# Kernel tuning notes

Measured on AMD Instinct MI355X. Metric: run time of the kernel, lower is better.

The kernel has to match this reference:

```python
import jax, jax.numpy as jnp
import numpy as np

N, E = 20000, 320000
IN, HID, R, HEADS = 128, 256, 4, 4
C = HID // HEADS  # per-head dim


def setup_inputs() -> dict:
    key = jax.random.key(0)
    ks = jax.random.split(key, 20)
    g = lambda k, s, sc=0.05: jax.random.normal(k, s, jnp.float32) * sc
    return {
        'x': g(ks[0], (N, IN), 1.0),
        'edge_index': jax.random.randint(ks[1], (2, E), 0, N),
        'edge_type': jax.random.randint(ks[2], (E,), 0, R),
        'h_prev': g(ks[3], (N, HID), 1.0),
        # RGCN layer 1: relation weights, root weight, bias
        'W1': g(ks[4], (R, IN, HID)), 'root1': g(ks[5], (IN, HID)), 'b1': jnp.zeros((HID,), jnp.float32),
        # RGCN layer 2
        'W2': g(ks[6], (R, HID, HID)), 'root2': g(ks[7], (HID, HID)), 'b2': jnp.zeros((HID,), jnp.float32),
        # TransformerConv linears (query/key/value/skip), each Linear(HID, HEADS*C)
        'Wq': g(ks[8], (HID, HID)), 'bq': jnp.zeros((HID,), jnp.float32),
        'Wk': g(ks[9], (HID, HID)), 'bk': jnp.zeros((HID,), jnp.float32),
        'Wv': g(ks[10], (HID, HID)), 'bv': jnp.zeros((HID,), jnp.float32),
        'Wskip': g(ks[11], (HID, HID)), 'bskip': jnp.zeros((HID,), jnp.float32),
        # GRUCell (torch layout: [3*HID, in], gates ordered r, z, n)
        'W_ih': g(ks[12], (3 * HID, HID)), 'b_ih': jnp.zeros((3 * HID,), jnp.float32),
        'W_hh': g(ks[13], (3 * HID, HID)), 'b_hh': jnp.zeros((3 * HID,), jnp.float32),
    }


def rgcn(x, src, dst, etype, W, Wroot, b):
    # PyG RGCNConv: out_i = x_i @ Wroot + b + sum_r mean_{j in N_r(i)} x_j @ W_r
    n = x.shape[0]
    out = x @ Wroot + b
    xs = x[src]  # [E, F_in]
    for r in range(W.shape[0]):  # small fixed relation count
        mask = (etype == r).astype(x.dtype)  # [E]
        msg = (xs @ W[r]) * mask[:, None]  # [E, F_out]
        agg = jax.ops.segment_sum(msg, dst, num_segments=n)
        cnt = jax.ops.segment_sum(mask, dst, num_segments=n)
        out = out + agg / jnp.maximum(cnt, 1.0)[:, None]
    return out


def transformer_conv(x, src, dst, Wq, bq, Wk, bk, Wv, bv, Wskip, bskip):
    # PyG TransformerConv, concat=True, root_weight=True
    n = x.shape[0]
    q = (x @ Wq + bq).reshape(n, HEADS, C)
    k = (x @ Wk + bk).reshape(n, HEADS, C)
    v = (x @ Wv + bv).reshape(n, HEADS, C)
    score = jnp.einsum('ehc,ehc->eh', q[dst], k[src]) * (1.0 / np.sqrt(C))  # [E, H]
    smax = jax.ops.segment_max(score, dst, num_segments=n)  # [N, H]
    ex = jnp.exp(score - smax[dst])
    denom = jax.ops.segment_sum(ex, dst, num_segments=n)
    alpha = ex / jnp.maximum(denom[dst], 1e-16)  # edge softmax per dst node
    out = jax.ops.segment_sum(alpha[:, :, None] * v[src], dst, num_segments=n)  # [N, H, C]
    return out.reshape(n, HEADS * C) + x @ Wskip + bskip


def gru_cell(xi, h, W_ih, b_ih, W_hh, b_hh):
    gi = xi @ W_ih.T + b_ih
    gh = h @ W_hh.T + b_hh
    ir, iz, inn = jnp.split(gi, 3, axis=1)
    hr, hz, hn = jnp.split(gh, 3, axis=1)
    r = jax.nn.sigmoid(ir + hr)
    z = jax.nn.sigmoid(iz + hz)
    nw = jnp.tanh(inn + r * hn)
    return (1.0 - z) * nw + z * h


def reference(x, edge_index, edge_type, h_prev, W1, root1, b1, W2, root2, b2,
              Wq, bq, Wk, bk, Wv, bv, Wskip, bskip, W_ih, b_ih, W_hh, b_hh):
    src, dst = edge_index[0], edge_index[1]
    h = jax.nn.relu(rgcn(x, src, dst, edge_type, W1, root1, b1))
    h = jax.nn.relu(rgcn(h, src, dst, edge_type, W2, root2, b2))
    h = transformer_conv(h, src, dst, Wq, bq, Wk, bk, Wv, bv, Wskip, bskip)
    h = gru_cell(h, h_prev, W_ih, b_ih, W_hh, b_hh)
    return h
```

## Files before the change

### kernel.cpp

```cpp
#include <hip/hip_runtime.h>
#include <hip/hip_bf16.h>
#include <stdint.h>

#define N_NODES 20000
#define E_EDGES 320000
#define IN_F    128
#define HIDF    256
#define R_REL   4
#define NRKEYS  (N_NODES*R_REL)
#define SCAN_BLOCKS 80
#define LDSP    40

typedef __attribute__((ext_vector_type(8))) short  short8;
typedef __attribute__((ext_vector_type(4))) float  floatx4;

__device__ __forceinline__ float bf2f(__hip_bfloat16 v){ return __bfloat162float(v); }
__device__ __forceinline__ __hip_bfloat16 f2bf(float v){ return __float2bfloat16(v); }
__device__ __forceinline__ float bfbits2f(unsigned short u){ return __uint_as_float(((unsigned)u)<<16); }
__device__ __forceinline__ unsigned short f2bfbits(float v){
    __hip_bfloat16 h = __float2bfloat16(v);
    return *(unsigned short*)&h;
}
__device__ __forceinline__ unsigned pack_bf2(float a, float b){
    return (unsigned)f2bfbits(a) | ((unsigned)f2bfbits(b) << 16);
}

__global__ void count_kernel(const int* __restrict__ ei, const int* __restrict__ et,
                             int* __restrict__ cnt)
{
    int e = blockIdx.x*256 + threadIdx.x;
    if (e >= E_EDGES) return;
    int dst = ei[E_EDGES + e];
    atomicAdd(&cnt[dst*R_REL + et[e]], 1);
}

__global__ __launch_bounds__(1024) void scan_reduce_kernel(const int* __restrict__ cnt,
                                                           int* __restrict__ blocksum)
{
    int ix = blockIdx.x*1024 + threadIdx.x;
    int v = (ix < NRKEYS) ? cnt[ix] : 0;
    #pragma unroll
    for (int o=32;o>0;o>>=1) v += __shfl_xor(v, o, 64);
    __shared__ int wsum[16];
    int wave = threadIdx.x >> 6, lane = threadIdx.x & 63;
    if (lane == 0) wsum[wave] = v;
    __syncthreads();
    if (threadIdx.x == 0) {
        int s = 0;
        #pragma unroll
        for (int w=0;w<16;w++) s += wsum[w];
        blocksum[blockIdx.x] = s;
    }
}

__global__ __launch_bounds__(128) void scan_sums_kernel(const int* __restrict__ blocksum,
                                                        int* __restrict__ blockoff)
{
    __shared__ int s[128];
    int t = threadIdx.x;
    int v = (t < SCAN_BLOCKS) ? blocksum[t] : 0;
    s[t] = v; __syncthreads();
    for (int off=1; off<128; off<<=1) {
        int u = (t>=off) ? s[t-off] : 0;
        __syncthreads();
        s[t] += u;
        __syncthreads();
    }
    if (t < SCAN_BLOCKS) blockoff[t] = s[t] - v;
}

__global__ __launch_bounds__(1024) void scan_apply_kernel(const int* __restrict__ cnt,
                                                          const int* __restrict__ blockoff,
                                                          int* __restrict__ row_ptr,
                                                          int* __restrict__ cursor)
{
    __shared__ int s[1024];
    int t = threadIdx.x;
    int ix = blockIdx.x*1024 + t;
    int v = (ix < NRKEYS) ? cnt[ix] : 0;
    s[t] = v; __syncthreads();
    for (int off=1; off<1024; off<<=1) {
        int u = (t>=off) ? s[t-off] : 0;
        __syncthreads();
        s[t] += u;
        __syncthreads();
    }
    if (ix < NRKEYS) {
        int excl = blockoff[blockIdx.x] + s[t] - v;
        row_ptr[ix] = excl;
        cursor[ix]  = excl;
        if (ix == NRKEYS-1) row_ptr[NRKEYS] = excl + v;
    }
}

__global__ void fill_kernel(const int* __restrict__ ei, const int* __restrict__ et,
                            int* __restrict__ cursor, int* __restrict__ csr_src)
{
    int e = blockIdx.x*256 + threadIdx.x;
    if (e >= E_EDGES) return;
    int src = ei[e];
    int dst = ei[E_EDGES + e];
    int key = dst*R_REL + et[e];
    int pos = atomicAdd(&cursor[key], 1);
    csr_src[pos] = src;
}

__global__ void make_b1t(const float* __restrict__ root1,
                         const float* __restrict__ W1,
                         __hip_bfloat16* __restrict__ B1t)
{
    int idx = blockIdx.x*256 + threadIdx.x;
    if (idx >= 256*640) return;
    int n = idx / 640, k = idx % 640;
    float v;
    if (k < 128) v = root1[k*256 + n];
    else         v = W1[(k-128)*256 + n];
    B1t[idx] = f2bf(v);
}

__global__ void make_b2t(const float* __restrict__ root2,
                         const float* __restrict__ W2,
                         __hip_bfloat16* __restrict__ B2t)
{
    int idx = blockIdx.x*256 + threadIdx.x;
    if (idx >= 256*1280) return;
    int n = idx / 1280, k = idx % 1280;
    float v;
    if (k < 256) v = root2[k*256 + n];
    else         v = W2[(k-256)*256 + n];
    B2t[idx] = f2bf(v);
}

__global__ void make_b3t(const float* __restrict__ Wq, const float* __restrict__ Wk,
                         const float* __restrict__ Wv, const float* __restrict__ Wsk,
                         const float* __restrict__ bq, const float* __restrict__ bk,
                         const float* __restrict__ bv, const float* __restrict__ bsk,
                         __hip_bfloat16* __restrict__ B3t, float* __restrict__ bias3)
{
    int idx = blockIdx.x*256 + threadIdx.x;
    if (idx >= 1024*256) return;
    int n = idx / 256, k = idx % 256;
    int g = n >> 8, nn = n & 255;
    const float* W = (g==0)?Wq:(g==1)?Wk:(g==2)?Wv:Wsk;
    B3t[idx] = f2bf(W[k*256 + nn]);
    if (k == 0) {
        const float* B = (g==0)?bq:(g==1)?bk:(g==2)?bv:bsk;
        bias3[n] = B[nn];
    }
}

__global__ void cvt_f32_bf16(const float* __restrict__ in, __hip_bfloat16* __restrict__ out, int n)
{
    int i = blockIdx.x*256 + threadIdx.x;
    if (i < n) out[i] = f2bf(in[i]);
}

__global__ __launch_bounds__(256) void agg1_kernel(const float* __restrict__ x,
                                                   const int* __restrict__ row_ptr,
                                                   const int* __restrict__ csr_src,
                                                   __hip_bfloat16* __restrict__ A1)
{
    int b = blockIdx.x*4 + (threadIdx.x >> 6);
    int lane = threadIdx.x & 63;
    int i = b >> 2, r = b & 3;
    int e0 = row_ptr[b], e1 = row_ptr[b+1];
    float sx0=0.f,sy0=0.f, sx1=0.f,sy1=0.f, sx2=0.f,sy2=0.f, sx3=0.f,sy3=0.f;
    int e = e0;
    for (; e+4 <= e1; e += 4) {
        int i0=csr_src[e], i1=csr_src[e+1], i2=csr_src[e+2], i3=csr_src[e+3];
        float2 v0 = *(const float2*)(x + (size_t)i0*IN_F + lane*2);
        float2 v1 = *(const float2*)(x + (size_t)i1*IN_F + lane*2);
        float2 v2 = *(const float2*)(x + (size_t)i2*IN_F + lane*2);
        float2 v3 = *(const float2*)(x + (size_t)i3*IN_F + lane*2);
        sx0+=v0.x; sy0+=v0.y; sx1+=v1.x; sy1+=v1.y;
        sx2+=v2.x; sy2+=v2.y; sx3+=v3.x; sy3+=v3.y;
    }
    for (; e < e1; e++) {
        int i0 = csr_src[e];
        float2 v = *(const float2*)(x + (size_t)i0*IN_F + lane*2);
        sx0+=v.x; sy0+=v.y;
    }
    float sx = (sx0+sx1)+(sx2+sx3);
    float sy = (sy0+sy1)+(sy2+sy3);
    float inv = (e1>e0) ? 1.f/(float)(e1-e0) : 0.f;
    *(unsigned*)(A1 + (size_t)i*640 + 128 + r*128 + lane*2) = pack_bf2(sx*inv, sy*inv);
    if (r == 0) {
        float2 v = *(const float2*)(x + (size_t)i*IN_F + lane*2);
        *(unsigned*)(A1 + (size_t)i*640 + lane*2) = pack_bf2(v.x, v.y);
    }
}

__global__ __launch_bounds__(256) void agg2_kernel(const int* __restrict__ row_ptr,
                                                   const int* __restrict__ csr_src,
                                                   __hip_bfloat16* __restrict__ A2)
{
    int b = blockIdx.x*4 + (threadIdx.x >> 6);
    int lane = threadIdx.x & 63;
    int i = b >> 2, r = b & 3;
    int e0 = row_ptr[b], e1 = row_ptr[b+1];
    float a0=0.f,a1=0.f,a2=0.f,a3=0.f;
    float b0=0.f,b1=0.f,b2=0.f,b3=0.f;
    float c0=0.f,c1=0.f,c2=0.f,c3=0.f;
    float d0=0.f,d1=0.f,d2=0.f,d3=0.f;
    int e = e0;
    for (; e+4 <= e1; e += 4) {
        int i0=csr_src[e], i1=csr_src[e+1], i2=csr_src[e+2], i3=csr_src[e+3];
        ushort4 u0 = *(const ushort4*)(A2 + (size_t)i0*1280 + lane*4);
        ushort4 u1 = *(const ushort4*)(A2 + (size_t)i1*1280 + lane*4);
        ushort4 u2 = *(const ushort4*)(A2 + (size_t)i2*1280 + lane*4);
        ushort4 u3 = *(const ushort4*)(A2 + (size_t)i3*1280 + lane*4);
        a0+=bfbits2f(u0.x); a1+=bfbits2f(u0.y); a2+=bfbits2f(u0.z); a3+=bfbits2f(u0.w);
        b0+=bfbits2f(u1.x); b1+=bfbits2f(u1.y); b2+=bfbits2f(u1.z); b3+=bfbits2f(u1.w);
        c0+=bfbits2f(u2.x); c1+=bfbits2f(u2.y); c2+=bfbits2f(u2.z); c3+=bfbits2f(u2.w);
        d0+=bfbits2f(u3.x); d1+=bfbits2f(u3.y); d2+=bfbits2f(u3.z); d3+=bfbits2f(u3.w);
    }
    for (; e < e1; e++) {
        int i0 = csr_src[e];
        ushort4 u = *(const ushort4*)(A2 + (size_t)i0*1280 + lane*4);
        a0+=bfbits2f(u.x); a1+=bfbits2f(u.y); a2+=bfbits2f(u.z); a3+=bfbits2f(u.w);
    }
    float s0=(a0+b0)+(c0+d0), s1=(a1+b1)+(c1+d1), s2=(a2+b2)+(c2+d2), s3=(a3+b3)+(c3+d3);
    float inv = (e1>e0) ? 1.f/(float)(e1-e0) : 0.f;
    uint2 w;
    w.x = pack_bf2(s0*inv, s1*inv);
    w.y = pack_bf2(s2*inv, s3*inv);
    *(uint2*)(A2 + (size_t)i*1280 + 256 + r*256 + lane*4) = w;
}

__device__ __forceinline__ void gemm_bt_body(const __hip_bfloat16* __restrict__ A, int lda,
                                             const __hip_bfloat16* __restrict__ Bt,
                                             const float* __restrict__ bias,
                                             __hip_bfloat16* __restrict__ C, int ldc,
                                             int M, int K, int relu,
                                             int tile_m, int tile_n,
                                             __hip_bfloat16* lds_a, __hip_bfloat16* lds_b)
{
    const int tid    = threadIdx.x;
    const int wave   = tid >> 6;
    const int lane   = tid & 63;
    const int wm = wave >> 1, wn = wave & 1;
    const int fm = lane & 15;
    const int q  = lane >> 4;

    floatx4 acc[4][4];
    #pragma unroll
    for (int i=0;i<4;i++)
        #pragma unroll
        for (int j=0;j<4;j++) acc[i][j] = (floatx4){0.f,0.f,0.f,0.f};

    const int srow   = tid >> 2;
    const int schunk = (tid & 3) * 8;
    const int ga0 = min(tile_m + srow,      M-1);
    const int ga1 = min(tile_m + 64 + srow, M-1);
    const __hip_bfloat16* arow0 = A  + (size_t)ga0*lda + schunk;
    const __hip_bfloat16* arow1 = A  + (size_t)ga1*lda + schunk;
    const __hip_bfloat16* brow0 = Bt + (size_t)(tile_n + srow)*K      + schunk;
    const __hip_bfloat16* brow1 = Bt + (size_t)(tile_n + 64 + srow)*K + schunk;

    uint4 pa0 = *(const uint4*)(arow0);
    uint4 pa1 = *(const uint4*)(arow1);
    uint4 pb0 = *(const uint4*)(brow0);
    uint4 pb1 = *(const uint4*)(brow1);

    for (int k0 = 0; k0 < K; k0 += 32) {
        __syncthreads();
        *(uint4*)(&lds_a[srow*LDSP      + schunk]) = pa0;
        *(uint4*)(&lds_a[(64+srow)*LDSP + schunk]) = pa1;
        *(uint4*)(&lds_b[srow*LDSP      + schunk]) = pb0;
        *(uint4*)(&lds_b[(64+srow)*LDSP + schunk]) = pb1;
        __syncthreads();

        int kn = k0 + 32;
        if (kn < K) {
            pa0 = *(const uint4*)(arow0 + kn);
            pa1 = *(const uint4*)(arow1 + kn);
            pb0 = *(const uint4*)(brow0 + kn);
            pb1 = *(const uint4*)(brow1 + kn);
        }

        short8 afr[4], bfr[4];
        #pragma unroll
        for (int i=0;i<4;i++) {
            afr[i] = *(const short8*)(&lds_a[(wm*64 + i*16 + fm)*LDSP + q*8]);
            bfr[i] = *(const short8*)(&lds_b[(wn*64 + i*16 + fm)*LDSP + q*8]);
        }
        #pragma unroll
        for (int i=0;i<4;i++)
            #pragma unroll
            for (int j=0;j<4;j++)
                acc[i][j] = __builtin_amdgcn_mfma_f32_16x16x32_bf16(afr[i], bfr[j], acc[i][j], 0,0,0);
    }

    const int crow_base = tile_m + wm*64;
    const int ccol_base = tile_n + wn*64;
    #pragma unroll
    for (int i=0;i<4;i++) {
        #pragma unroll
        for (int j=0;j<4;j++) {
            int c  = ccol_base + j*16 + fm;
            float bb = bias[c];
            #pragma unroll
            for (int rg=0; rg<4; rg++) {
                int r = crow_base + i*16 + q*4 + rg;
                if (r < M) {
                    float v = acc[i][j][rg] + bb;
                    if (relu) v = fmaxf(v, 0.f);
                    C[(size_t)r*ldc + c] = f2bf(v);
                }
            }
        }
    }
}

__global__ __launch_bounds__(256) void gemm_bt(const __hip_bfloat16* __restrict__ A, int lda,
                                               const __hip_bfloat16* __restrict__ Bt,
                                               const float* __restrict__ bias,
                                               __hip_bfloat16* __restrict__ C, int ldc,
                                               int M, int K, int relu)
{
    __shared__ __align__(16) __hip_bfloat16 lds_a[128*LDSP];
    __shared__ __align__(16) __hip_bfloat16 lds_b[128*LDSP];
    gemm_bt_body(A, lda, Bt, bias, C, ldc, M, K, relu,
                 blockIdx.x*128, blockIdx.y*128, lds_a, lds_b);
}

__global__ __launch_bounds__(256) void gemm_bt_dual(const __hip_bfloat16* __restrict__ A0,
                                                    const __hip_bfloat16* __restrict__ A1,
                                                    const __hip_bfloat16* __restrict__ Bt0,
                                                    const __hip_bfloat16* __restrict__ Bt1,
                                                    const float* __restrict__ bias0,
                                                    const float* __restrict__ bias1,
                                                    __hip_bfloat16* __restrict__ C0,
                                                    __hip_bfloat16* __restrict__ C1)
{
    __shared__ __align__(16) __hip_bfloat16 lds_a[128*LDSP];
    __shared__ __align__(16) __hip_bfloat16 lds_b[128*LDSP];
    int which = blockIdx.y >= 6;
    int ty    = which ? (blockIdx.y - 6) : blockIdx.y;
    gemm_bt_body(which ? A1 : A0, 256,
                 which ? Bt1 : Bt0,
                 which ? bias1 : bias0,
                 which ? C1 : C0, 768,
                 N_NODES, 256, 0,
                 blockIdx.x*128, ty*128, lds_a, lds_b);
}

__global__ __launch_bounds__(256) void score_kernel(const __hip_bfloat16* __restrict__ qkvs,
                                                    const int* __restrict__ row_ptr,
                                                    const int* __restrict__ csr_src,
                                                    float* __restrict__ score)
{
    int i = blockIdx.x*4 + (threadIdx.x >> 6);
    int lane = threadIdx.x & 63;
    int h = lane >> 4, d4 = lane & 15;
    int e0 = row_ptr[i*R_REL], e1 = row_ptr[i*R_REL + R_REL];
    ushort4 qv = *(const ushort4*)(qkvs + (size_t)i*1024 + lane*4);
    float qx=bfbits2f(qv.x), qy=bfbits2f(qv.y), qz=bfbits2f(qv.z), qw=bfbits2f(qv.w);
    float* sp = score + (size_t)h*E_EDGES;
    int j = e0;
    for (; j+2 <= e1; j += 2) {
        int s0 = csr_src[j], s1 = csr_src[j+1];
        ushort4 k0 = *(const ushort4*)(qkvs + (size_t)s0*1024 + 256 + lane*4);
        ushort4 k1 = *(const ushort4*)(qkvs + (size_t)s1*1024 + 256 + lane*4);
        float d0 = qx*bfbits2f(k0.x)+qy*bfbits2f(k0.y)+qz*bfbits2f(k0.z)+qw*bfbits2f(k0.w);
        float d1 = qx*bfbits2f(k1.x)+qy*bfbits2f(k1.y)+qz*bfbits2f(k1.z)+qw*bfbits2f(k1.w);
        #pragma unroll
        for (int o=1;o<16;o<<=1){ d0 += __shfl_xor(d0,o,64); d1 += __shfl_xor(d1,o,64); }
        if (d4 == 0) { sp[j] = d0*0.125f; sp[j+1] = d1*0.125f; }
    }
    for (; j < e1; j++) {
        int s0 = csr_src[j];
        ushort4 k0 = *(const ushort4*)(qkvs + (size_t)s0*1024 + 256 + lane*4);
        float d0 = qx*bfbits2f(k0.x)+qy*bfbits2f(k0.y)+qz*bfbits2f(k0.z)+qw*bfbits2f(k0.w);
        #pragma unroll
        for (int o=1;o<16;o<<=1) d0 += __shfl_xor(d0,o,64);
        if (d4 == 0) sp[j] = d0*0.125f;
    }
}

__global__ __launch_bounds__(256) void attn_agg_kernel(const __hip_bfloat16* __restrict__ qkvs,
                                                       const float* __restrict__ score,
                                                       const int* __restrict__ row_ptr,
                                                       const int* __restrict__ csr_src,
                                                       __hip_bfloat16* __restrict__ hatt)
{
    int i = blockIdx.x*4 + (threadIdx.x >> 6);
    int lane = threadIdx.x & 63;
    int h  = lane >> 4;
    int d4 = lane & 15;
    int e0 = row_ptr[i*R_REL], e1 = row_ptr[i*R_REL + R_REL];
    int deg = e1 - e0;
    const float* sp = score + (size_t)h*E_EDGES + e0;

    float m = -1e30f;
    for (int j = d4; j < deg; j += 16) m = fmaxf(m, sp[j]);
    #pragma unroll
    for (int o=1;o<16;o<<=1) m = fmaxf(m, __shfl_xor(m, o, 64));

    float ssum = 0.f;
    for (int j = d4; j < deg; j += 16) ssum += __expf(sp[j] - m);
    #pragma unroll
    for (int o=1;o<16;o<<=1) ssum += __shfl_xor(ssum, o, 64);
    float inv = 1.f / fmaxf(ssum, 1e-16f);

    float ax=0.f, ay=0.f, az=0.f, aw=0.f;
    int j = 0;
    for (; j+4 <= deg; j += 4) {
        int s0=csr_src[e0+j], s1=csr_src[e0+j+1], s2=csr_src[e0+j+2], s3=csr_src[e0+j+3];
        float w0 = __expf(sp[j]   - m) * inv;
        float w1 = __expf(sp[j+1] - m) * inv;
        float w2 = __expf(sp[j+2] - m) * inv;
        float w3 = __expf(sp[j+3] - m) * inv;
        ushort4 u0 = *(const ushort4*)(qkvs + (size_t)s0*1024 + 512 + lane*4);
        ushort4 u1 = *(const ushort4*)(qkvs + (size_t)s1*1024 + 512 + lane*4);
        ushort4 u2 = *(const ushort4*)(qkvs + (size_t)s2*1024 + 512 + lane*4);
        ushort4 u3 = *(const ushort4*)(qkvs + (size_t)s3*1024 + 512 + lane*4);
        ax += w0*bfbits2f(u0.x) + w1*bfbits2f(u1.x) + w2*bfbits2f(u2.x) + w3*bfbits2f(u3.x);
        ay += w0*bfbits2f(u0.y) + w1*bfbits2f(u1.y) + w2*bfbits2f(u2.y) + w3*bfbits2f(u3.y);
        az += w0*bfbits2f(u0.z) + w1*bfbits2f(u1.z) + w2*bfbits2f(u2.z) + w3*bfbits2f(u3.z);
        aw += w0*bfbits2f(u0.w) + w1*bfbits2f(u1.w) + w2*bfbits2f(u2.w) + w3*bfbits2f(u3.w);
    }
    for (; j < deg; j++) {
        int s = csr_src[e0+j];
        float w = __expf(sp[j] - m) * inv;
        ushort4 u = *(const ushort4*)(qkvs + (size_t)s*1024 + 512 + lane*4);
        ax += w*bfbits2f(u.x); ay += w*bfbits2f(u.y);
        az += w*bfbits2f(u.z); aw += w*bfbits2f(u.w);
    }
    ushort4 sk = *(const ushort4*)(qkvs + (size_t)i*1024 + 768 + lane*4);
    uint2 w;
    w.x = pack_bf2(ax + bfbits2f(sk.x), ay + bfbits2f(sk.y));
    w.y = pack_bf2(az + bfbits2f(sk.z), aw + bfbits2f(sk.w));
    *(uint2*)(hatt + (size_t)i*256 + lane*4) = w;
}

__global__ void gru_kernel(const __hip_bfloat16* __restrict__ gi,
                           const __hip_bfloat16* __restrict__ gh,
                           const float* __restrict__ hprev,
                           float* __restrict__ out)
{
    int idx = blockIdx.x*256 + threadIdx.x;
    if (idx >= N_NODES*HIDF) return;
    int i = idx / HIDF, c = idx % HIDF;
    size_t gb = (size_t)i*768;
    float ir = bf2f(gi[gb + c]), iz = bf2f(gi[gb + 256 + c]), in = bf2f(gi[gb + 512 + c]);
    float hr = bf2f(gh[gb + c]), hz = bf2f(gh[gb + 256 + c]), hn = bf2f(gh[gb + 512 + c]);
    float r = 1.f/(1.f + __expf(-(ir+hr)));
    float z = 1.f/(1.f + __expf(-(iz+hz)));
    float n = tanhf(in + r*hn);
    float h = hprev[idx];
    out[idx] = (1.f - z)*n + z*h;
}

extern "C" void kernel_launch(void* const* d_in, const int* in_sizes, int n_in,
                              void* d_out, int out_size, void* d_ws, size_t ws_size,
                              hipStream_t stream)
{
    const float* x       = (const float*)d_in[0];
    const int* edge_index= (const int*)d_in[1];
    const int* edge_type = (const int*)d_in[2];
    const float* hprev   = (const float*)d_in[3];
    const float* W1      = (const float*)d_in[4];
    const float* root1   = (const float*)d_in[5];
    const float* b1      = (const float*)d_in[6];
    const float* W2      = (const float*)d_in[7];
    const float* root2   = (const float*)d_in[8];
    const float* b2      = (const float*)d_in[9];
    const float* Wq      = (const float*)d_in[10];
    const float* bq      = (const float*)d_in[11];
    const float* Wk      = (const float*)d_in[12];
    const float* bk      = (const float*)d_in[13];
    const float* Wv      = (const float*)d_in[14];
    const float* bv      = (const float*)d_in[15];
    const float* Wskip   = (const float*)d_in[16];
    const float* bskip   = (const float*)d_in[17];
    const float* W_ih    = (const float*)d_in[18];
    const float* b_ih    = (const float*)d_in[19];
    const float* W_hh    = (const float*)d_in[20];
    const float* b_hh    = (const float*)d_in[21];

    char* ws = (char*)d_ws;
    size_t off = 0;
    auto take = [&](size_t bytes)->char* {
        char* p = ws + off;
        off = (off + bytes + 255) & ~(size_t)255;
        return p;
    };
    int* cnt        = (int*)take((size_t)NRKEYS*4);
    int* row_ptr    = (int*)take((size_t)(NRKEYS+1)*4);
    int* cursor     = (int*)take((size_t)NRKEYS*4);
    int* csr_src    = (int*)take((size_t)E_EDGES*4);
    int* blocksum   = (int*)take((size_t)SCAN_BLOCKS*4);
    int* blockoff   = (int*)take((size_t)(SCAN_BLOCKS+1)*4);
    float* score    = (float*)take((size_t)R_REL*E_EDGES*4);
    __hip_bfloat16* B1t   = (__hip_bfloat16*)take((size_t)256*640*2);
    __hip_bfloat16* B2t   = (__hip_bfloat16*)take((size_t)256*1280*2);
    __hip_bfloat16* B3t   = (__hip_bfloat16*)take((size_t)1024*256*2);
    __hip_bfloat16* Biht  = (__hip_bfloat16*)take((size_t)768*256*2);
    __hip_bfloat16* Bhht  = (__hip_bfloat16*)take((size_t)768*256*2);
    float*          bias3 = (float*)take((size_t)1024*4);
    __hip_bfloat16* hprev_bf = (__hip_bfloat16*)take((size_t)N_NODES*256*2);
    char* P1 = take((size_t)N_NODES*640*2);
    char* P2 = take((size_t)N_NODES*1536*2);

    __hip_bfloat16* A1   = (__hip_bfloat16*)P1;
    __hip_bfloat16* h2   = (__hip_bfloat16*)P1;
    __hip_bfloat16* hatt = (__hip_bfloat16*)P1;
    __hip_bfloat16* A2   = (__hip_bfloat16*)P2;
    __hip_bfloat16* qkvs = (__hip_bfloat16*)P2;
    __hip_bfloat16* gi   = (__hip_bfloat16*)P2;
    __hip_bfloat16* gh   = (__hip_bfloat16*)(P2 + (size_t)N_NODES*768*2);

    hipMemsetAsync(cnt, 0, (size_t)NRKEYS*4, stream);
    count_kernel<<<(E_EDGES+255)/256, 256, 0, stream>>>(edge_index, edge_type, cnt);
    scan_reduce_kernel<<<SCAN_BLOCKS, 1024, 0, stream>>>(cnt, blocksum);
    scan_sums_kernel<<<1, 128, 0, stream>>>(blocksum, blockoff);
    scan_apply_kernel<<<SCAN_BLOCKS, 1024, 0, stream>>>(cnt, blockoff, row_ptr, cursor);
    fill_kernel<<<(E_EDGES+255)/256, 256, 0, stream>>>(edge_index, edge_type, cursor, csr_src);

    make_b1t<<<(256*640+255)/256, 256, 0, stream>>>(root1, W1, B1t);
    make_b2t<<<(256*1280+255)/256, 256, 0, stream>>>(root2, W2, B2t);
    make_b3t<<<(1024*256+255)/256, 256, 0, stream>>>(Wq, Wk, Wv, Wskip, bq, bk, bv, bskip, B3t, bias3);
    cvt_f32_bf16<<<(768*256+255)/256, 256, 0, stream>>>(W_ih, Biht, 768*256);
    cvt_f32_bf16<<<(768*256+255)/256, 256, 0, stream>>>(W_hh, Bhht, 768*256);
    cvt_f32_bf16<<<(N_NODES*256+255)/256, 256, 0, stream>>>(hprev, hprev_bf, N_NODES*256);

    agg1_kernel<<<NRKEYS/4, 256, 0, stream>>>(x, row_ptr, csr_src, A1);

    dim3 g12(157, 2);
    gemm_bt<<<g12, 256, 0, stream>>>(A1, 640, B1t, b1, A2, 1280, N_NODES, 640, 1);

    agg2_kernel<<<NRKEYS/4, 256, 0, stream>>>(row_ptr, csr_src, A2);

    gemm_bt<<<g12, 256, 0, stream>>>(A2, 1280, B2t, b2, h2, 256, N_NODES, 1280, 1);

    dim3 g3(157, 8);
    gemm_bt<<<g3, 256, 0, stream>>>(h2, 256, B3t, bias3, qkvs, 1024, N_NODES, 256, 0);

    score_kernel<<<N_NODES/4, 256, 0, stream>>>(qkvs, row_ptr, csr_src, score);
    attn_agg_kernel<<<N_NODES/4, 256, 0, stream>>>(qkvs, score, row_ptr, csr_src, hatt);

    dim3 g45(157, 12);
    gemm_bt_dual<<<g45, 256, 0, stream>>>(hatt, hprev_bf, Biht, Bhht, b_ih, b_hh, gi, gh);

    gru_kernel<<<(N_NODES*HIDF+255)/256, 256, 0, stream>>>(gi, gh, hprev, (float*)d_out);
}
```

Measured before the change: 451.1 us.

## Double-buffer GEMM tiles via direct global-to-LDS loads with swizzle and smaller M tiles

Rewrites the shared GEMM body so tiles are loaded straight from global memory into LDS with global_load_lds, into two LDS buffers, which lets the next K-slice load overlap the MFMA work on the current one. The LDS layout drops the old padding in favour of an XOR swizzle to avoid bank conflicts. The tile M size becomes a template parameter, and the two RGCN GEMMs use 64-row tiles to double the block count on a grid that was only 314 blocks. The costs are more LDS per block, a full vmcnt(0) wait each iteration, and the correctness of the swizzle and per-wave row mapping.

```diff
diff --git a/kernel.cpp b/kernel.cpp
--- a/kernel.cpp
+++ b/kernel.cpp
@@ -9,7 +9,6 @@
 #define R_REL   4
 #define NRKEYS  (N_NODES*R_REL)
 #define SCAN_BLOCKS 80
-#define LDSP    40
 
 typedef __attribute__((ext_vector_type(8))) short  short8;
 typedef __attribute__((ext_vector_type(4))) float  floatx4;
@@ -23,6 +22,12 @@
 }
 __device__ __forceinline__ unsigned pack_bf2(float a, float b){
     return (unsigned)f2bfbits(a) | ((unsigned)f2bfbits(b) << 16);
+}
+
+__device__ __forceinline__ void gload_lds16(const void* g, void* l)
+{
+    __builtin_amdgcn_global_load_lds((const __attribute__((address_space(1))) void*)g,
+                                     (__attribute__((address_space(3))) void*)l, 16, 0, 0);
 }
 
 __global__ void count_kernel(const int* __restrict__ ei, const int* __restrict__ et,
@@ -227,6 +232,7 @@
     *(uint2*)(A2 + (size_t)i*1280 + 256 + r*256 + lane*4) = w;
 }
 
+template<int MI>
 __device__ __forceinline__ void gemm_bt_body(const __hip_bfloat16* __restrict__ A, int lda,
                                              const __hip_bfloat16* __restrict__ Bt,
                                              const float* __restrict__ bias,
@@ -235,66 +241,89 @@
                                              int tile_m, int tile_n,
                                              __hip_bfloat16* lds_a, __hip_bfloat16* lds_b)
 {
-    const int tid    = threadIdx.x;
-    const int wave   = tid >> 6;
-    const int lane   = tid & 63;
+    constexpr int A_ELEMS = MI*1024;
+    const int tid  = threadIdx.x;
+    const int wave = tid >> 6;
+    const int lane = tid & 63;
     const int wm = wave >> 1, wn = wave & 1;
     const int fm = lane & 15;
     const int q  = lane >> 4;
-
-    floatx4 acc[4][4];
-    #pragma unroll
-    for (int i=0;i<4;i++)
+    const int sw = (q ^ ((fm >> 1) & 3)) * 8;
+
+    floatx4 acc[MI][4];
+    #pragma unroll
+    for (int i=0;i<MI;i++)
         #pragma unroll
         for (int j=0;j<4;j++) acc[i][j] = (floatx4){0.f,0.f,0.f,0.f};
 
-    const int srow   = tid >> 2;
-    const int schunk = (tid & 3) * 8;
-    const int ga0 = min(tile_m + srow,      M-1);
-    const int ga1 = min(tile_m + 64 + srow, M-1);
-    const __hip_bfloat16* arow0 = A  + (size_t)ga0*lda + schunk;
-    const __hip_bfloat16* arow1 = A  + (size_t)ga1*lda + schunk;
-    const __hip_bfloat16* brow0 = Bt + (size_t)(tile_n + srow)*K      + schunk;
-    const __hip_bfloat16* brow1 = Bt + (size_t)(tile_n + 64 + srow)*K + schunk;
-
-    uint4 pa0 = *(const uint4*)(arow0);
-    uint4 pa1 = *(const uint4*)(arow1);
-    uint4 pb0 = *(const uint4*)(brow0);
-    uint4 pb1 = *(const uint4*)(brow1);
-
-    for (int k0 = 0; k0 < K; k0 += 32) {
-        __syncthreads();
-        *(uint4*)(&lds_a[srow*LDSP      + schunk]) = pa0;
-        *(uint4*)(&lds_a[(64+srow)*LDSP + schunk]) = pa1;
-        *(uint4*)(&lds_b[srow*LDSP      + schunk]) = pb0;
-        *(uint4*)(&lds_b[(64+srow)*LDSP + schunk]) = pb1;
-        __syncthreads();
-
-        int kn = k0 + 32;
-        if (kn < K) {
-            pa0 = *(const uint4*)(arow0 + kn);
-            pa1 = *(const uint4*)(arow1 + kn);
-            pb0 = *(const uint4*)(brow0 + kn);
-            pb1 = *(const uint4*)(brow1 + kn);
+    const int srow   = lane >> 2;
+    const int schunk = lane & 3;
+    size_t a_goff[MI/2];  __hip_bfloat16* a_ldst[MI/2];
+    #pragma unroll
+    for (int s = 0; s < MI/2; ++s) {
+        int r = (s*4 + wave)*16 + srow;
+        int c = schunk ^ ((r >> 1) & 3);
+        a_goff[s] = (size_t)min(tile_m + r, M-1)*lda + c*8;
+        a_ldst[s] = lds_a + (s*4 + wave)*512;
+    }
+    size_t b_goff[2];  __hip_bfloat16* b_ldst[2];
+    #pragma unroll
+    for (int s = 0; s < 2; ++s) {
+        int r = (s*4 + wave)*16 + srow;
+        int c = schunk ^ ((r >> 1) & 3);
+        b_goff[s] = (size_t)(tile_n + r)*K + c*8;
+        b_ldst[s] = lds_b + (s*4 + wave)*512;
+    }
+
+    const int nt = K >> 5;
+
+    #pragma unroll
+    for (int s = 0; s < MI/2; ++s) gload_lds16(A + a_goff[s], a_ldst[s]);
+    #pragma unroll
+    for (int s = 0; s < 2; ++s)    gload_lds16(Bt + b_goff[s], b_ldst[s]);
+    asm volatile("s_waitcnt vmcnt(0)" ::: "memory");
+    __builtin_amdgcn_s_barrier();
+
+    int cur = 0;
+    for (int t = 0; t < nt; ++t) {
+        if (t + 1 < nt) {
+            const int nb = cur ^ 1;
+            const int kn = (t + 1) << 5;
+            #pragma unroll
+            for (int s = 0; s < MI/2; ++s)
+                gload_lds16(A + a_goff[s] + kn, a_ldst[s] + nb*A_ELEMS);
+            #pragma unroll
+            for (int s = 0; s < 2; ++s)
+                gload_lds16(Bt + b_goff[s] + kn, b_ldst[s] + nb*4096);
         }
 
-        short8 afr[4], bfr[4];
-        #pragma unroll
-        for (int i=0;i<4;i++) {
-            afr[i] = *(const short8*)(&lds_a[(wm*64 + i*16 + fm)*LDSP + q*8]);
-            bfr[i] = *(const short8*)(&lds_b[(wn*64 + i*16 + fm)*LDSP + q*8]);
-        }
-        #pragma unroll
-        for (int i=0;i<4;i++)
+        const __hip_bfloat16* la = lds_a + cur*A_ELEMS;
+        const __hip_bfloat16* lb = lds_b + cur*4096;
+        short8 afr[MI], bfr[4];
+        #pragma unroll
+        for (int i=0;i<MI;i++)
+            afr[i] = *(const short8*)(la + (wm*(MI*16) + i*16 + fm)*32 + sw);
+        #pragma unroll
+        for (int j=0;j<4;j++)
+            bfr[j] = *(const short8*)(lb + (wn*64 + j*16 + fm)*32 + sw);
+
+        #pragma unroll
+        for (int i=0;i<MI;i++)
             #pragma unroll
             for (int j=0;j<4;j++)
                 acc[i][j] = __builtin_amdgcn_mfma_f32_16x16x32_bf16(afr[i], bfr[j], acc[i][j], 0,0,0);
-    }
-
-    const int crow_base = tile_m + wm*64;
+
+        if (t + 1 < nt) {
+            asm volatile("s_waitcnt vmcnt(0)" ::: "memory");
+            __builtin_amdgcn_s_barrier();
+            cur ^= 1;
+        }
+    }
+
+    const int crow_base = tile_m + wm*(MI*16);
     const int ccol_base = tile_n + wn*64;
     #pragma unroll
-    for (int i=0;i<4;i++) {
+    for (int i=0;i<MI;i++) {
         #pragma unroll
         for (int j=0;j<4;j++) {
             int c  = ccol_base + j*16 + fm;
@@ -312,16 +341,17 @@
     }
 }
 
-__global__ __launch_bounds__(256) void gemm_bt(const __hip_bfloat16* __restrict__ A, int lda,
-                                               const __hip_bfloat16* __restrict__ Bt,
-                                               const float* __restrict__ bias,
-                                               __hip_bfloat16* __restrict__ C, int ldc,
-                                               int M, int K, int relu)
-{
-    __shared__ __align__(16) __hip_bfloat16 lds_a[128*LDSP];
-    __shared__ __align__(16) __hip_bfloat16 lds_b[128*LDSP];
-    gemm_bt_body(A, lda, Bt, bias, C, ldc, M, K, relu,
-                 blockIdx.x*128, blockIdx.y*128, lds_a, lds_b);
+template<int MI>
+__global__ __launch_bounds__(256) void gemm_bt_t(const __hip_bfloat16* __restrict__ A, int lda,
+                                                 const __hip_bfloat16* __restrict__ Bt,
+                                                 const float* __restrict__ bias,
+                                                 __hip_bfloat16* __restrict__ C, int ldc,
+                                                 int M, int K, int relu)
+{
+    __shared__ __align__(16) __hip_bfloat16 lds_a[2*MI*1024];
+    __shared__ __align__(16) __hip_bfloat16 lds_b[2*4096];
+    gemm_bt_body<MI>(A, lda, Bt, bias, C, ldc, M, K, relu,
+                     blockIdx.x*(MI*32), blockIdx.y*128, lds_a, lds_b);
 }
 
 __global__ __launch_bounds__(256) void gemm_bt_dual(const __hip_bfloat16* __restrict__ A0,
@@ -333,16 +363,16 @@
                                                     __hip_bfloat16* __restrict__ C0,
                                                     __hip_bfloat16* __restrict__ C1)
 {
-    __shared__ __align__(16) __hip_bfloat16 lds_a[128*LDSP];
-    __shared__ __align__(16) __hip_bfloat16 lds_b[128*LDSP];
+    __shared__ __align__(16) __hip_bfloat16 lds_a[2*4096];
+    __shared__ __align__(16) __hip_bfloat16 lds_b[2*4096];
     int which = blockIdx.y >= 6;
     int ty    = which ? (blockIdx.y - 6) : blockIdx.y;
-    gemm_bt_body(which ? A1 : A0, 256,
-                 which ? Bt1 : Bt0,
-                 which ? bias1 : bias0,
-                 which ? C1 : C0, 768,
-                 N_NODES, 256, 0,
-                 blockIdx.x*128, ty*128, lds_a, lds_b);
+    gemm_bt_body<4>(which ? A1 : A0, 256,
+                    which ? Bt1 : Bt0,
+                    which ? bias1 : bias0,
+                    which ? C1 : C0, 768,
+                    N_NODES, 256, 0,
+                    blockIdx.x*128, ty*128, lds_a, lds_b);
 }
 
 __global__ __launch_bounds__(256) void score_kernel(const __hip_bfloat16* __restrict__ qkvs,
@@ -527,15 +557,15 @@
 
     agg1_kernel<<<NRKEYS/4, 256, 0, stream>>>(x, row_ptr, csr_src, A1);
 
-    dim3 g12(157, 2);
-    gemm_bt<<<g12, 256, 0, stream>>>(A1, 640, B1t, b1, A2, 1280, N_NODES, 640, 1);
+    dim3 g12(313, 2);
+    gemm_bt_t<2><<<g12, 256, 0, stream>>>(A1, 640, B1t, b1, A2, 1280, N_NODES, 640, 1);
 
     agg2_kernel<<<NRKEYS/4, 256, 0, stream>>>(row_ptr, csr_src, A2);
 
-    gemm_bt<<<g12, 256, 0, stream>>>(A2, 1280, B2t, b2, h2, 256, N_NODES, 1280, 1);
+    gemm_bt_t<2><<<g12, 256, 0, stream>>>(A2, 1280, B2t, b2, h2, 256, N_NODES, 1280, 1);
 
     dim3 g3(157, 8);
-    gemm_bt<<<g3, 256, 0, stream>>>(h2, 256, B3t, bias3, qkvs, 1024, N_NODES, 256, 0);
+    gemm_bt_t<4><<<g3, 256, 0, stream>>>(h2, 256, B3t, bias3, qkvs, 1024, N_NODES, 256, 0);
 
     score_kernel<<<N_NODES/4, 256, 0, stream>>>(qkvs, row_ptr, csr_src, score);
     attn_agg_kernel<<<N_NODES/4, 256, 0, stream>>>(qkvs, score, row_ptr, csr_src, hatt);
```

New measurement: 450.5 us. Within noise of the previous version (-0.1%).
